# Kernel tuning notes

Measured on AMD Instinct MI355X. Metric: run time of the kernel, lower is better.

Reference implementation:

```python
import jax, jax.numpy as jnp
import numpy as np
import math

# Constants matching init_kwargs
H = 16            # num_attention_heads
K = 8             # tisa_num_kernels
NUM_AGNOSTIC = 2  # num_position_agnostic_heads
MAX_FV = 512.0
MIN_FV = 8.0
P_EPS = 1e-8
EPS = 1e-8


def _slopes():
    # ALiBi-like geometric slope schedule from the module __init__ (non-learned buffer)
    first = -math.log(P_EPS) / (MIN_FV / 2.0)
    last = -math.log(P_EPS) / (MAX_FV / 2.0)
    aware = H - NUM_AGNOSTIC
    s = first * (last / first) ** (jnp.arange(H, dtype=jnp.float32) / (aware - 1))
    # position-agnostic heads get zero slope
    return s * (jnp.arange(H) < aware).astype(jnp.float32)


def setup_inputs() -> dict:
    key = jax.random.key(0)
    ks = jax.random.split(key, 5)
    B, L, D = 4, 1024, 64
    q = jax.random.normal(ks[0], (B, H, L, D), jnp.float32)
    k = jax.random.normal(ks[1], (B, H, L, D), jnp.float32)
    v = jax.random.normal(ks[2], (B, H, L, D), jnp.float32)
    offsets = jax.random.normal(ks[3], (1, K, H, 1, 1), jnp.float32) * 15.0
    amplitudes = jax.random.normal(ks[4], (1, K, H, 1, 1), jnp.float32) * 0.01
    sharpness = jnp.full((1, K, H, 1, 1), 5.0, jnp.float32)
    bias_param = jnp.ones((1, H, 1, 1), jnp.float32)
    return {"q": q, "k": k, "v": v, "offsets": offsets, "amplitudes": amplitudes,
            "sharpness": sharpness, "bias_param": bias_param}


def reference(q, k, v, offsets, amplitudes, sharpness, bias_param):
    B, Hh, L, D = q.shape
    rel = jnp.arange(-L + 1, L, dtype=q.dtype)            # (2L-1,) relative positions
    slopes = _slopes()                                     # (H,)
    exp_decay = -jnp.abs(rel)[None, :] * slopes[:, None]   # (H, 2L-1)

    off = offsets.reshape(K, Hh, 1)
    amp = amplitudes.reshape(K, Hh, 1)
    sh = sharpness.reshape(K, Hh, 1)
    # sigmoid kernel per (kernel, head, relpos); eval mode -> no dropout
    kernel = jnp.abs(amp) * jax.nn.sigmoid(jnp.sign(amp) * ((rel[None, None, :] - off) / sh))
    ksum = kernel.sum(axis=0)                              # (H, 2L-1)
    bias_rel = jnp.log(ksum + EPS + bias_param.reshape(Hh, 1))
    rel_bias = bias_rel + exp_decay                        # (H, 2L-1)

    # relative -> absolute: bias[i, j] = rel_bias[j - i + L - 1]
    idx = jnp.arange(L)[None, :] - jnp.arange(L)[:, None] + (L - 1)  # (L, L)
    attn_bias = rel_bias[:, idx]                           # (H, L, L)

    scale = 1.0 / jnp.sqrt(jnp.asarray(D, q.dtype))
    scores = jnp.einsum('bhqd,bhkd->bhqk', q, k) * scale + attn_bias[None]
    probs = jax.nn.softmax(scores, axis=-1)
    return jnp.einsum('bhqk,bhkd->bhqd', probs, v)
```

## Files before the change

### kernel.cpp

```cpp
#include <hip/hip_runtime.h>
#include <math.h>

#define Bq 4
#define Hh 16
#define Lq 1024
#define Dd 64
#define Kk 8
#define QT 128
#define KT 64
#define SRk 72
#define TB 1152
#define FMAX 8.0f
#define LOG2E 1.44269504f

typedef __attribute__((ext_vector_type(8))) short short8;
typedef __attribute__((ext_vector_type(4))) short short4v;
typedef __attribute__((ext_vector_type(16))) float f32x16;

__device__ __forceinline__ short f2bf(float x) {
    unsigned u = __float_as_uint(x);
    u += 0x7FFFu + ((u >> 16) & 1u);
    return (short)(u >> 16);
}

__device__ __forceinline__ int jperm(int j) {
    return (j & 32) | ((j & 8) << 1) | ((j & 4) << 1) | ((j & 16) >> 2) | (j & 3);
}

__global__ __launch_bounds__(256) void attn_kernel(
    const float* __restrict__ qp, const float* __restrict__ kp,
    const float* __restrict__ vp,
    const float* __restrict__ off, const float* __restrict__ amp,
    const float* __restrict__ sh, const float* __restrict__ bpar,
    float* __restrict__ out)
{
    __shared__ __align__(16) short k_s[KT * SRk];
    __shared__ __align__(16) short v_s[Dd * SRk];
    __shared__ __align__(16) float bias4[4 * TB];
    __shared__ float l_s[QT];

    const int bh = blockIdx.x;
    const int qs = blockIdx.y * QT;
    const int t  = threadIdx.x;
    const int w  = t >> 6;
    const int lane = t & 63;
    const int l31 = lane & 31;
    const int h5  = lane >> 5;
    const int h   = bh & 15;

    float slope = (h < Hh - 2) ? 4.605170185988092f * exp2f(-6.0f * (float)h / 13.0f) : 0.0f;
    #pragma unroll
    for (int it = 0; it < 5; ++it) {
        int i = it * 256 + t;
        if (i < TB - 1) {
            float rel = (float)(i - 127 - qs);
            float ksum = 0.0f;
            #pragma unroll
            for (int kk = 0; kk < Kk; ++kk) {
                float a = amp[kk * Hh + h];
                float o = off[kk * Hh + h];
                float s = sh[kk * Hh + h];
                float sgn = (a > 0.0f) ? 1.0f : ((a < 0.0f) ? -1.0f : 0.0f);
                ksum += fabsf(a) / (1.0f + __expf(-sgn * (rel - o) / s));
            }
            bias4[i] = (logf(ksum + 1e-8f + bpar[h]) - fabsf(rel) * slope - FMAX) * LOG2E;
        }
    }

    const float QS = 0.125f * LOG2E;
    short8 bq[4];
    const float* qrow = qp + ((size_t)bh * Lq + qs + 32 * w + l31) * Dd;
    #pragma unroll
    for (int c = 0; c < 4; ++c) {
        float4 x0 = *(const float4*)(qrow + c * 16 + h5 * 8);
        float4 x1 = *(const float4*)(qrow + c * 16 + h5 * 8 + 4);
        short8 a;
        a[0]=f2bf(x0.x*QS); a[1]=f2bf(x0.y*QS); a[2]=f2bf(x0.z*QS); a[3]=f2bf(x0.w*QS);
        a[4]=f2bf(x1.x*QS); a[5]=f2bf(x1.y*QS); a[6]=f2bf(x1.z*QS); a[7]=f2bf(x1.w*QS);
        bq[c] = a;
    }

    const float* kbase = kp + (size_t)bh * Lq * Dd;
    const float* vbase = vp + (size_t)bh * Lq * Dd;
    int srow[4], scol4[4], svcol[4];
    #pragma unroll
    for (int it = 0; it < 4; ++it) {
        int fi = it * 256 + t;
        srow[it]  = fi >> 4;
        scol4[it] = (fi & 15) * 4;
        svcol[it] = jperm(srow[it]) ^ (8 * ((scol4[it] >> 3) & 7));
    }

    float4 kreg[4], vreg[4];
    #pragma unroll
    for (int it = 0; it < 4; ++it) {
        kreg[it] = *(const float4*)(kbase + (size_t)srow[it] * Dd + scol4[it]);
        vreg[it] = *(const float4*)(vbase + (size_t)srow[it] * Dd + scol4[it]);
    }

    __syncthreads();

    #pragma unroll
    for (int it = 0; it < 5; ++it) {
        int i = it * 256 + t;
        if (i < TB) {
            float b1 = bias4[i + 1 <= TB - 2 ? i + 1 : TB - 2];
            float b2 = bias4[i + 2 <= TB - 2 ? i + 2 : TB - 2];
            float b3 = bias4[i + 3 <= TB - 2 ? i + 3 : TB - 2];
            bias4[TB + i]     = b1;
            bias4[2 * TB + i] = b2;
            bias4[3 * TB + i] = b3;
        }
    }
    #pragma unroll
    for (int it = 0; it < 4; ++it) {
        short4v k4;
        k4[0]=f2bf(kreg[it].x); k4[1]=f2bf(kreg[it].y); k4[2]=f2bf(kreg[it].z); k4[3]=f2bf(kreg[it].w);
        *(short4v*)&k_s[srow[it] * SRk + scol4[it]] = k4;
        v_s[(scol4[it] + 0) * SRk + svcol[it]] = f2bf(vreg[it].x);
        v_s[(scol4[it] + 1) * SRk + svcol[it]] = f2bf(vreg[it].y);
        v_s[(scol4[it] + 2) * SRk + svcol[it]] = f2bf(vreg[it].z);
        v_s[(scol4[it] + 3) * SRk + svcol[it]] = f2bf(vreg[it].w);
    }
    __syncthreads();

    f32x16 O0, O1;
    #pragma unroll
    for (int r = 0; r < 16; ++r) { O0[r] = 0.f; O1[r] = 0.f; }
    float l_part = 0.0f;

    const int L0 = 4 * h5 - 32 * w - l31 + 127;
    const int phi = L0 & 3;
    const float* bcopy = bias4 + phi * TB - phi;

    #pragma unroll 1
    for (int kt = 0; kt < Lq / KT; ++kt) {
        const int ks = kt * KT;

        if (kt < 15) {
            const float* kn = kbase + (size_t)(ks + KT) * Dd;
            const float* vn = vbase + (size_t)(ks + KT) * Dd;
            #pragma unroll
            for (int it = 0; it < 4; ++it) {
                kreg[it] = *(const float4*)(kn + (size_t)srow[it] * Dd + scol4[it]);
                vreg[it] = *(const float4*)(vn + (size_t)srow[it] * Dd + scol4[it]);
            }
        }

        f32x16 S0, S1;
        #pragma unroll
        for (int r = 0; r < 16; ++r) { S0[r] = 0.f; S1[r] = 0.f; }
        #pragma unroll
        for (int c = 0; c < 4; ++c) {
            short8 ak0 = *(const short8*)&k_s[(l31) * SRk + c * 16 + h5 * 8];
            S0 = __builtin_amdgcn_mfma_f32_32x32x16_bf16(ak0, bq[c], S0, 0, 0, 0);
        }
        #pragma unroll
        for (int c = 0; c < 4; ++c) {
            short8 ak1 = *(const short8*)&k_s[(32 + l31) * SRk + c * 16 + h5 * 8];
            S1 = __builtin_amdgcn_mfma_f32_32x32x16_bf16(ak1, bq[c], S1, 0, 0, 0);
        }

        float lsum = 0.0f;
        #pragma unroll
        for (int p = 0; p < 4; ++p) {
            int base0 = ks + 8 * p + L0;
            float4 b0 = *(const float4*)(bcopy + base0);
            float4 b1 = *(const float4*)(bcopy + base0 + 32);
            #pragma unroll
            for (int q = 0; q < 4; ++q) {
                int r = 4 * p + q;
                float bq0 = (q == 0) ? b0.x : (q == 1) ? b0.y : (q == 2) ? b0.z : b0.w;
                float bq1 = (q == 0) ? b1.x : (q == 1) ? b1.y : (q == 2) ? b1.z : b1.w;
                float e0 = __builtin_amdgcn_exp2f(S0[r] + bq0);
                float e1 = __builtin_amdgcn_exp2f(S1[r] + bq1);
                S0[r] = e0; S1[r] = e1;
                lsum += e0 + e1;
            }
        }
        l_part += lsum;

        short8 ap[4];
        #pragma unroll
        for (int c = 0; c < 4; ++c) {
            short8 a;
            #pragma unroll
            for (int s = 0; s < 8; ++s) {
                int r = (c & 1) * 4 + (s & 3) + 8 * (s >> 2);
                a[s] = f2bf((c >> 1) ? S1[r] : S0[r]);
            }
            ap[c] = a;
        }

        #pragma unroll
        for (int nb = 0; nb < 2; ++nb) {
            int d = nb * 32 + l31;
            int swzr = 8 * ((d >> 3) & 7);
            f32x16 acc = nb ? O1 : O0;
            #pragma unroll
            for (int c = 0; c < 4; ++c) {
                short8 bv = *(const short8*)&v_s[d * SRk + ((c * 16 + h5 * 8) ^ swzr)];
                acc = __builtin_amdgcn_mfma_f32_32x32x16_bf16(ap[c], bv, acc, 0, 0, 0);
            }
            if (nb) O1 = acc; else O0 = acc;
        }

        __syncthreads();
        if (kt < 15) {
            #pragma unroll
            for (int it = 0; it < 4; ++it) {
                short4v k4;
                k4[0]=f2bf(kreg[it].x); k4[1]=f2bf(kreg[it].y); k4[2]=f2bf(kreg[it].z); k4[3]=f2bf(kreg[it].w);
                *(short4v*)&k_s[srow[it] * SRk + scol4[it]] = k4;
                v_s[(scol4[it] + 0) * SRk + svcol[it]] = f2bf(vreg[it].x);
                v_s[(scol4[it] + 1) * SRk + svcol[it]] = f2bf(vreg[it].y);
                v_s[(scol4[it] + 2) * SRk + svcol[it]] = f2bf(vreg[it].z);
                v_s[(scol4[it] + 3) * SRk + svcol[it]] = f2bf(vreg[it].w);
            }
        }
        __syncthreads();
    }

    float l = l_part;
    l += __shfl_xor(l, 32);
    l_s[32 * w + l31] = 1.0f / l;
    float* ob = out + ((size_t)bh * Lq + qs) * Dd;
    #pragma unroll
    for (int r = 0; r < 16; ++r) {
        int rowp = (r & 3) + 8 * (r >> 2) + 4 * h5;
        float inv = l_s[32 * w + rowp];
        ob[(size_t)(32 * w + rowp) * Dd + l31]      = O0[r] * inv;
        ob[(size_t)(32 * w + rowp) * Dd + 32 + l31] = O1[r] * inv;
    }
}

extern "C" void kernel_launch(void* const* d_in, const int* in_sizes, int n_in,
                              void* d_out, int out_size, void* d_ws, size_t ws_size,
                              hipStream_t stream) {
    const float* q   = (const float*)d_in[0];
    const float* k   = (const float*)d_in[1];
    const float* v   = (const float*)d_in[2];
    const float* off = (const float*)d_in[3];
    const float* amp = (const float*)d_in[4];
    const float* sh  = (const float*)d_in[5];
    const float* bp  = (const float*)d_in[6];
    float* out = (float*)d_out;

    dim3 grid(Bq * Hh, Lq / QT);
    attn_kernel<<<grid, 256, 0, stream>>>(q, k, v, off, amp, sh, bp, out);
}
```

Before: 131.8 us.

## Double key tile to 128, vectorize V transpose stores, cheaper bf16 rounding

Raises the key/value tile from 64 to 128 rows so each iteration processes two 64-wide sub-tiles, halving the number of barrier pairs and LDS refill phases. Loads are reorganized so each thread holds 4 consecutive rows, letting V be transposed into LDS with 4-element vector stores instead of scalar stores. The bf16 conversion switches from round-to-nearest-even to a simpler round-half-up, and launch bounds request 2 blocks per CU. The prefetch registers and LDS use both double, which raises register pressure and may limit occupancy.

Result: faster. 126.1 us (-4.3%).

```diff
diff --git a/kernel.cpp b/kernel.cpp
--- a/kernel.cpp
+++ b/kernel.cpp
@@ -7,8 +7,9 @@
 #define Dd 64
 #define Kk 8
 #define QT 128
-#define KT 64
+#define KT 128
 #define SRk 72
+#define SRv 136
 #define TB 1152
 #define FMAX 8.0f
 #define LOG2E 1.44269504f
@@ -17,17 +18,15 @@
 typedef __attribute__((ext_vector_type(4))) short short4v;
 typedef __attribute__((ext_vector_type(16))) float f32x16;
 
-__device__ __forceinline__ short f2bf(float x) {
-    unsigned u = __float_as_uint(x);
-    u += 0x7FFFu + ((u >> 16) & 1u);
-    return (short)(u >> 16);
+__device__ __forceinline__ short f2bh(float x) {
+    return (short)((__float_as_uint(x) + 0x8000u) >> 16);
 }
 
 __device__ __forceinline__ int jperm(int j) {
     return (j & 32) | ((j & 8) << 1) | ((j & 4) << 1) | ((j & 16) >> 2) | (j & 3);
 }
 
-__global__ __launch_bounds__(256) void attn_kernel(
+__global__ __launch_bounds__(256, 2) void attn_kernel(
     const float* __restrict__ qp, const float* __restrict__ kp,
     const float* __restrict__ vp,
     const float* __restrict__ off, const float* __restrict__ amp,
@@ -35,7 +34,7 @@
     float* __restrict__ out)
 {
     __shared__ __align__(16) short k_s[KT * SRk];
-    __shared__ __align__(16) short v_s[Dd * SRk];
+    __shared__ __align__(16) short v_s[Dd * SRv];
     __shared__ __align__(16) float bias4[4 * TB];
     __shared__ float l_s[QT];
 
@@ -75,28 +74,27 @@
         float4 x0 = *(const float4*)(qrow + c * 16 + h5 * 8);
         float4 x1 = *(const float4*)(qrow + c * 16 + h5 * 8 + 4);
         short8 a;
-        a[0]=f2bf(x0.x*QS); a[1]=f2bf(x0.y*QS); a[2]=f2bf(x0.z*QS); a[3]=f2bf(x0.w*QS);
-        a[4]=f2bf(x1.x*QS); a[5]=f2bf(x1.y*QS); a[6]=f2bf(x1.z*QS); a[7]=f2bf(x1.w*QS);
+        a[0]=f2bh(x0.x*QS); a[1]=f2bh(x0.y*QS); a[2]=f2bh(x0.z*QS); a[3]=f2bh(x0.w*QS);
+        a[4]=f2bh(x1.x*QS); a[5]=f2bh(x1.y*QS); a[6]=f2bh(x1.z*QS); a[7]=f2bh(x1.w*QS);
         bq[c] = a;
     }
 
+    const int g  = t >> 4;
+    const int cl = t & 15;
+    const int j0 = 4 * g;
+    const int c4 = 4 * cl;
+    const int vcb[2] = { jperm(j0), 64 + jperm(j0) };
     const float* kbase = kp + (size_t)bh * Lq * Dd;
     const float* vbase = vp + (size_t)bh * Lq * Dd;
-    int srow[4], scol4[4], svcol[4];
-    #pragma unroll
-    for (int it = 0; it < 4; ++it) {
-        int fi = it * 256 + t;
-        srow[it]  = fi >> 4;
-        scol4[it] = (fi & 15) * 4;
-        svcol[it] = jperm(srow[it]) ^ (8 * ((scol4[it] >> 3) & 7));
-    }
-
-    float4 kreg[4], vreg[4];
-    #pragma unroll
-    for (int it = 0; it < 4; ++it) {
-        kreg[it] = *(const float4*)(kbase + (size_t)srow[it] * Dd + scol4[it]);
-        vreg[it] = *(const float4*)(vbase + (size_t)srow[it] * Dd + scol4[it]);
-    }
+
+    float4 kr[2][4], vr[2][4];
+    #pragma unroll
+    for (int s = 0; s < 2; ++s)
+        #pragma unroll
+        for (int u = 0; u < 4; ++u) {
+            kr[s][u] = *(const float4*)(kbase + (size_t)(64 * s + j0 + u) * Dd + c4);
+            vr[s][u] = *(const float4*)(vbase + (size_t)(64 * s + j0 + u) * Dd + c4);
+        }
 
     __syncthreads();
 
@@ -113,14 +111,25 @@
         }
     }
     #pragma unroll
-    for (int it = 0; it < 4; ++it) {
-        short4v k4;
-        k4[0]=f2bf(kreg[it].x); k4[1]=f2bf(kreg[it].y); k4[2]=f2bf(kreg[it].z); k4[3]=f2bf(kreg[it].w);
-        *(short4v*)&k_s[srow[it] * SRk + scol4[it]] = k4;
-        v_s[(scol4[it] + 0) * SRk + svcol[it]] = f2bf(vreg[it].x);
-        v_s[(scol4[it] + 1) * SRk + svcol[it]] = f2bf(vreg[it].y);
-        v_s[(scol4[it] + 2) * SRk + svcol[it]] = f2bf(vreg[it].z);
-        v_s[(scol4[it] + 3) * SRk + svcol[it]] = f2bf(vreg[it].w);
+    for (int s = 0; s < 2; ++s) {
+        #pragma unroll
+        for (int u = 0; u < 4; ++u) {
+            short4v k4;
+            k4[0]=f2bh(kr[s][u].x); k4[1]=f2bh(kr[s][u].y);
+            k4[2]=f2bh(kr[s][u].z); k4[3]=f2bh(kr[s][u].w);
+            *(short4v*)&k_s[(64 * s + j0 + u) * SRk + c4] = k4;
+        }
+        #pragma unroll
+        for (int cc = 0; cc < 4; ++cc) {
+            int d = c4 + cc;
+            float e0 = ((const float*)&vr[s][0])[cc];
+            float e1 = ((const float*)&vr[s][1])[cc];
+            float e2 = ((const float*)&vr[s][2])[cc];
+            float e3 = ((const float*)&vr[s][3])[cc];
+            short4v v4;
+            v4[0]=f2bh(e0); v4[1]=f2bh(e1); v4[2]=f2bh(e2); v4[3]=f2bh(e3);
+            *(short4v*)&v_s[d * SRv + (vcb[s] ^ (8 * ((d >> 3) & 7)))] = v4;
+        }
     }
     __syncthreads();
 
@@ -137,85 +146,101 @@
     for (int kt = 0; kt < Lq / KT; ++kt) {
         const int ks = kt * KT;
 
-        if (kt < 15) {
+        if (kt < 7) {
             const float* kn = kbase + (size_t)(ks + KT) * Dd;
             const float* vn = vbase + (size_t)(ks + KT) * Dd;
             #pragma unroll
-            for (int it = 0; it < 4; ++it) {
-                kreg[it] = *(const float4*)(kn + (size_t)srow[it] * Dd + scol4[it]);
-                vreg[it] = *(const float4*)(vn + (size_t)srow[it] * Dd + scol4[it]);
-            }
-        }
-
-        f32x16 S0, S1;
-        #pragma unroll
-        for (int r = 0; r < 16; ++r) { S0[r] = 0.f; S1[r] = 0.f; }
-        #pragma unroll
-        for (int c = 0; c < 4; ++c) {
-            short8 ak0 = *(const short8*)&k_s[(l31) * SRk + c * 16 + h5 * 8];
-            S0 = __builtin_amdgcn_mfma_f32_32x32x16_bf16(ak0, bq[c], S0, 0, 0, 0);
-        }
-        #pragma unroll
-        for (int c = 0; c < 4; ++c) {
-            short8 ak1 = *(const short8*)&k_s[(32 + l31) * SRk + c * 16 + h5 * 8];
-            S1 = __builtin_amdgcn_mfma_f32_32x32x16_bf16(ak1, bq[c], S1, 0, 0, 0);
-        }
-
-        float lsum = 0.0f;
-        #pragma unroll
-        for (int p = 0; p < 4; ++p) {
-            int base0 = ks + 8 * p + L0;
-            float4 b0 = *(const float4*)(bcopy + base0);
-            float4 b1 = *(const float4*)(bcopy + base0 + 32);
-            #pragma unroll
-            for (int q = 0; q < 4; ++q) {
-                int r = 4 * p + q;
-                float bq0 = (q == 0) ? b0.x : (q == 1) ? b0.y : (q == 2) ? b0.z : b0.w;
-                float bq1 = (q == 0) ? b1.x : (q == 1) ? b1.y : (q == 2) ? b1.z : b1.w;
-                float e0 = __builtin_amdgcn_exp2f(S0[r] + bq0);
-                float e1 = __builtin_amdgcn_exp2f(S1[r] + bq1);
-                S0[r] = e0; S1[r] = e1;
-                lsum += e0 + e1;
-            }
-        }
-        l_part += lsum;
-
-        short8 ap[4];
-        #pragma unroll
-        for (int c = 0; c < 4; ++c) {
-            short8 a;
-            #pragma unroll
-            for (int s = 0; s < 8; ++s) {
-                int r = (c & 1) * 4 + (s & 3) + 8 * (s >> 2);
-                a[s] = f2bf((c >> 1) ? S1[r] : S0[r]);
-            }
-            ap[c] = a;
-        }
-
-        #pragma unroll
-        for (int nb = 0; nb < 2; ++nb) {
-            int d = nb * 32 + l31;
-            int swzr = 8 * ((d >> 3) & 7);
-            f32x16 acc = nb ? O1 : O0;
+            for (int s = 0; s < 2; ++s)
+                #pragma unroll
+                for (int u = 0; u < 4; ++u) {
+                    kr[s][u] = *(const float4*)(kn + (size_t)(64 * s + j0 + u) * Dd + c4);
+                    vr[s][u] = *(const float4*)(vn + (size_t)(64 * s + j0 + u) * Dd + c4);
+                }
+        }
+
+        #pragma unroll
+        for (int s = 0; s < 2; ++s) {
+            f32x16 S0, S1;
+            #pragma unroll
+            for (int r = 0; r < 16; ++r) { S0[r] = 0.f; S1[r] = 0.f; }
             #pragma unroll
             for (int c = 0; c < 4; ++c) {
-                short8 bv = *(const short8*)&v_s[d * SRk + ((c * 16 + h5 * 8) ^ swzr)];
-                acc = __builtin_amdgcn_mfma_f32_32x32x16_bf16(ap[c], bv, acc, 0, 0, 0);
-            }
-            if (nb) O1 = acc; else O0 = acc;
+                short8 ak0 = *(const short8*)&k_s[(64 * s + l31) * SRk + c * 16 + h5 * 8];
+                S0 = __builtin_amdgcn_mfma_f32_32x32x16_bf16(ak0, bq[c], S0, 0, 0, 0);
+            }
+            #pragma unroll
+            for (int c = 0; c < 4; ++c) {
+                short8 ak1 = *(const short8*)&k_s[(64 * s + 32 + l31) * SRk + c * 16 + h5 * 8];
+                S1 = __builtin_amdgcn_mfma_f32_32x32x16_bf16(ak1, bq[c], S1, 0, 0, 0);
+            }
+
+            float lsum = 0.0f;
+            #pragma unroll
+            for (int p = 0; p < 4; ++p) {
+                int base0 = ks + 64 * s + 8 * p + L0;
+                float4 b0 = *(const float4*)(bcopy + base0);
+                float4 b1 = *(const float4*)(bcopy + base0 + 32);
+                #pragma unroll
+                for (int q = 0; q < 4; ++q) {
+                    int r = 4 * p + q;
+                    float bq0 = (q == 0) ? b0.x : (q == 1) ? b0.y : (q == 2) ? b0.z : b0.w;
+                    float bq1 = (q == 0) ? b1.x : (q == 1) ? b1.y : (q == 2) ? b1.z : b1.w;
+                    float e0 = __builtin_amdgcn_exp2f(S0[r] + bq0);
+                    float e1 = __builtin_amdgcn_exp2f(S1[r] + bq1);
+                    S0[r] = e0; S1[r] = e1;
+                    lsum += e0 + e1;
+                }
+            }
+            l_part += lsum;
+
+            short8 ap[4];
+            #pragma unroll
+            for (int c = 0; c < 4; ++c) {
+                short8 a;
+                #pragma unroll
+                for (int e = 0; e < 8; ++e) {
+                    int r = (c & 1) * 4 + (e & 3) + 8 * (e >> 2);
+                    a[e] = f2bh((c >> 1) ? S1[r] : S0[r]);
+                }
+                ap[c] = a;
+            }
+
+            #pragma unroll
+            for (int nb = 0; nb < 2; ++nb) {
+                int d = nb * 32 + l31;
+                int swz = 8 * ((d >> 3) & 7);
+                f32x16 acc = nb ? O1 : O0;
+                #pragma unroll
+                for (int c = 0; c < 4; ++c) {
+                    short8 bv = *(const short8*)&v_s[d * SRv + 64 * s + ((c * 16 + h5 * 8) ^ swz)];
+                    acc = __builtin_amdgcn_mfma_f32_32x32x16_bf16(ap[c], bv, acc, 0, 0, 0);
+                }
+                if (nb) O1 = acc; else O0 = acc;
+            }
         }
 
         __syncthreads();
-        if (kt < 15) {
-            #pragma unroll
-            for (int it = 0; it < 4; ++it) {
-                short4v k4;
-                k4[0]=f2bf(kreg[it].x); k4[1]=f2bf(kreg[it].y); k4[2]=f2bf(kreg[it].z); k4[3]=f2bf(kreg[it].w);
-                *(short4v*)&k_s[srow[it] * SRk + scol4[it]] = k4;
-                v_s[(scol4[it] + 0) * SRk + svcol[it]] = f2bf(vreg[it].x);
-                v_s[(scol4[it] + 1) * SRk + svcol[it]] = f2bf(vreg[it].y);
-                v_s[(scol4[it] + 2) * SRk + svcol[it]] = f2bf(vreg[it].z);
-                v_s[(scol4[it] + 3) * SRk + svcol[it]] = f2bf(vreg[it].w);
+        if (kt < 7) {
+            #pragma unroll
+            for (int s = 0; s < 2; ++s) {
+                #pragma unroll
+                for (int u = 0; u < 4; ++u) {
+                    short4v k4;
+                    k4[0]=f2bh(kr[s][u].x); k4[1]=f2bh(kr[s][u].y);
+                    k4[2]=f2bh(kr[s][u].z); k4[3]=f2bh(kr[s][u].w);
+                    *(short4v*)&k_s[(64 * s + j0 + u) * SRk + c4] = k4;
+                }
+                #pragma unroll
+                for (int cc = 0; cc < 4; ++cc) {
+                    int d = c4 + cc;
+                    float e0 = ((const float*)&vr[s][0])[cc];
+                    float e1 = ((const float*)&vr[s][1])[cc];
+                    float e2 = ((const float*)&vr[s][2])[cc];
+                    float e3 = ((const float*)&vr[s][3])[cc];
+                    short4v v4;
+                    v4[0]=f2bh(e0); v4[1]=f2bh(e1); v4[2]=f2bh(e2); v4[3]=f2bh(e3);
+                    *(short4v*)&v_s[d * SRv + (vcb[s] ^ (8 * ((d >> 3) & 7)))] = v4;
+                }
             }
         }
         __syncthreads();
```
